# Optimization experiments

Hardware: AMD Instinct MI355X
Metric: run time of the kernel (lower is better)

The kernel has to match this reference:

```python
import jax, jax.numpy as jnp
import numpy as np

H = 512        # HIDDEN_SIZE
HEADS = 4      # MEM_HEAD
KDIM = 256     # K_DIM (= H//2), HEADS*KDIM == 2*H
HALF = KDIM // 2
KNN = 32
SUB = 512      # SUB_SIZE
MEM = SUB * SUB
BN_EPS = 1e-5


def setup_inputs() -> dict:
    key = jax.random.key(0)
    ks = jax.random.split(key, 6)
    x = jax.random.normal(ks[0], (32, 64, H), jnp.float32)
    w1 = jax.random.normal(ks[1], (H // 2, H), jnp.float32) / np.sqrt(H).astype(np.float32)
    b1 = jnp.zeros((H // 2,), jnp.float32)
    w2 = jax.random.normal(ks[2], (2 * H, H // 2), jnp.float32) / np.sqrt(H // 2).astype(np.float32)
    b2 = jnp.zeros((2 * H,), jnp.float32)
    bn_gamma = jnp.ones((KDIM,), jnp.float32)
    bn_beta = jnp.zeros((KDIM,), jnp.float32)
    keys = jax.random.normal(ks[3], (HEADS, 2, SUB, HALF), jnp.float32) / np.sqrt(HALF).astype(np.float32)
    values = jax.random.normal(ks[4], (MEM, H), jnp.float32) * (H ** -0.5)
    return dict(x=x, w1=w1, b1=b1, w2=w2, b2=b2,
                bn_gamma=bn_gamma, bn_beta=bn_beta, keys=keys, values=values)


def reference(x, w1, b1, w2, b2, bn_gamma, bn_beta, keys, values):
    B, L, _ = x.shape
    n = B * L
    # Query MLP: H -> H/2 -> 2H, viewed as (n, HEADS, KDIM)
    h = jax.nn.relu(jnp.einsum('blh,ch->blc', x, w1) + b1)
    q = jnp.einsum('blc,dc->bld', h, w2) + b2                      # (B, L, 2H)
    q = q.reshape(n, HEADS, KDIM)
    # BatchNorm1d over the K_DIM channel (training-mode batch stats)
    flat = q.reshape(-1, KDIM)
    mean = flat.mean(0)
    var = flat.var(0)
    q = (q - mean) * jax.lax.rsqrt(var + BN_EPS) * bn_gamma + bn_beta
    # Product-key double top-k
    q1, q2 = q[..., :HALF], q[..., HALF:]
    s1 = jnp.einsum('nhd,hkd->nhk', q1, keys[:, 0])                # (n, HEADS, SUB)
    s2 = jnp.einsum('nhd,hkd->nhk', q2, keys[:, 1])
    ts1, ti1 = jax.lax.top_k(s1, KNN)
    ts2, ti2 = jax.lax.top_k(s2, KNN)
    all_s = (ts1[..., :, None] + ts2[..., None, :]).reshape(n, HEADS, KNN * KNN)
    all_i = (ti1[..., :, None] * SUB + ti2[..., None, :]).reshape(n, HEADS, KNN * KNN)
    sc, best = jax.lax.top_k(all_s, KNN)                            # (n, HEADS, KNN)
    idx = jnp.take_along_axis(all_i, best, axis=-1)
    # Softmax over KNN within each head (scores viewed as (-1, KNN))
    w = jax.nn.softmax(sc, axis=-1)
    idx = idx.reshape(n, HEADS * KNN)
    w = w.reshape(n, HEADS * KNN)
    # EmbeddingBag(mode='sum') with per-sample weights
    out = jnp.einsum('nkh,nk->nh', values[idx], w)                  # (n, H)
    out = out.reshape(B, L, H)
    return out.sum(1)                                               # (B, H)
```

## Files before the change

### kernel.cpp

```cpp
#include <hip/hip_runtime.h>
#include <hip/hip_bf16.h>
#include <math.h>

#define N_TOK   2048
#define HDIM    512
#define HHALF   256
#define QDIM    1024
#define KDIM    256
#define HALF    128
#define HEADS   4
#define KNN     32
#define SUB     512
#define NROWS   8192

__device__ __forceinline__ void gemm_tile_nt(
    const float* __restrict__ A, int lda,
    const float* __restrict__ B, int ldb,
    float* __restrict__ C, int ldc,
    int K, const float* __restrict__ bias, bool relu,
    int m0, int n0)
{
    __shared__ float As[16][68];
    __shared__ float Bs[16][68];
    int tid = threadIdx.x;
    int tx = tid & 15;
    int ty = tid >> 4;
    int lr = tid >> 2;
    int lc = (tid & 3) * 4;

    float acc[4][4] = {};

    for (int k0 = 0; k0 < K; k0 += 16) {
        float4 a = *(const float4*)(A + (size_t)(m0 + lr) * lda + k0 + lc);
        float4 b = *(const float4*)(B + (size_t)(n0 + lr) * ldb + k0 + lc);
        As[lc + 0][lr] = a.x; As[lc + 1][lr] = a.y;
        As[lc + 2][lr] = a.z; As[lc + 3][lr] = a.w;
        Bs[lc + 0][lr] = b.x; Bs[lc + 1][lr] = b.y;
        Bs[lc + 2][lr] = b.z; Bs[lc + 3][lr] = b.w;
        __syncthreads();
#pragma unroll
        for (int k = 0; k < 16; ++k) {
            float4 av = *(const float4*)&As[k][ty * 4];
            float4 bv = *(const float4*)&Bs[k][tx * 4];
            acc[0][0] = fmaf(av.x, bv.x, acc[0][0]);
            acc[0][1] = fmaf(av.x, bv.y, acc[0][1]);
            acc[0][2] = fmaf(av.x, bv.z, acc[0][2]);
            acc[0][3] = fmaf(av.x, bv.w, acc[0][3]);
            acc[1][0] = fmaf(av.y, bv.x, acc[1][0]);
            acc[1][1] = fmaf(av.y, bv.y, acc[1][1]);
            acc[1][2] = fmaf(av.y, bv.z, acc[1][2]);
            acc[1][3] = fmaf(av.y, bv.w, acc[1][3]);
            acc[2][0] = fmaf(av.z, bv.x, acc[2][0]);
            acc[2][1] = fmaf(av.z, bv.y, acc[2][1]);
            acc[2][2] = fmaf(av.z, bv.z, acc[2][2]);
            acc[2][3] = fmaf(av.z, bv.w, acc[2][3]);
            acc[3][0] = fmaf(av.w, bv.x, acc[3][0]);
            acc[3][1] = fmaf(av.w, bv.y, acc[3][1]);
            acc[3][2] = fmaf(av.w, bv.z, acc[3][2]);
            acc[3][3] = fmaf(av.w, bv.w, acc[3][3]);
        }
        __syncthreads();
    }

    float4 bb = make_float4(0.f, 0.f, 0.f, 0.f);
    if (bias) {
        bb.x = bias[n0 + tx * 4 + 0];
        bb.y = bias[n0 + tx * 4 + 1];
        bb.z = bias[n0 + tx * 4 + 2];
        bb.w = bias[n0 + tx * 4 + 3];
    }
#pragma unroll
    for (int i = 0; i < 4; ++i) {
        int m = m0 + ty * 4 + i;
        float4 r;
        r.x = acc[i][0] + bb.x;
        r.y = acc[i][1] + bb.y;
        r.z = acc[i][2] + bb.z;
        r.w = acc[i][3] + bb.w;
        if (relu) {
            r.x = fmaxf(r.x, 0.f); r.y = fmaxf(r.y, 0.f);
            r.z = fmaxf(r.z, 0.f); r.w = fmaxf(r.w, 0.f);
        }
        *(float4*)(C + (size_t)m * ldc + n0 + tx * 4) = r;
    }
}

__global__ __launch_bounds__(256) void gemm_nt_kernel(
    const float* __restrict__ A, int lda,
    const float* __restrict__ B, int ldb,
    float* __restrict__ C, int ldc,
    int K, const float* __restrict__ bias, int relu)
{
    gemm_tile_nt(A, lda, B, ldb, C, ldc, K, bias, relu != 0,
                 blockIdx.x * 64, blockIdx.y * 64);
}

__global__ __launch_bounds__(256) void score_kernel(
    const float* __restrict__ q, const float* __restrict__ keys,
    float* __restrict__ s1, float* __restrict__ s2)
{
    int z = blockIdx.z;
    int hh = z >> 1;
    int half = z & 1;
    const float* A = q + hh * KDIM + half * HALF;
    const float* B = keys + (size_t)z * SUB * HALF;
    float* C = (half ? s2 : s1) + hh * SUB;
    gemm_tile_nt(A, QDIM, B, HALF, C, HEADS * SUB, HALF, nullptr, false,
                 blockIdx.x * 64, blockIdx.y * 64);
}

__global__ __launch_bounds__(256) void bnstat_kernel(
    const float* __restrict__ q, float* __restrict__ partial)
{
    int c = threadIdx.x;
    int b = blockIdx.x;
    const float* base = q + (size_t)b * 32 * KDIM;
    float s = 0.f, s2 = 0.f;
#pragma unroll 8
    for (int r = 0; r < 32; ++r) {
        float v = base[r * KDIM + c];
        s += v;
        s2 = fmaf(v, v, s2);
    }
    partial[b * KDIM + c] = s;
    partial[256 * KDIM + b * KDIM + c] = s2;
}

__global__ __launch_bounds__(256) void bnfinal_kernel(
    const float* __restrict__ partial,
    const float* __restrict__ gamma, const float* __restrict__ beta,
    float* __restrict__ scsh)
{
    int c = threadIdx.x;
    float s = 0.f, s2 = 0.f;
    for (int b = 0; b < 256; ++b) {
        s += partial[b * KDIM + c];
        s2 += partial[256 * KDIM + b * KDIM + c];
    }
    float mean = s * (1.f / (float)NROWS);
    float var = s2 * (1.f / (float)NROWS) - mean * mean;
    float rstd = rsqrtf(var + 1e-5f);
    float sc = rstd * gamma[c];
    scsh[c] = sc;
    scsh[KDIM + c] = beta[c] - mean * sc;
}

__global__ __launch_bounds__(256) void bnapply_kernel(
    float* __restrict__ q, const float* __restrict__ scsh)
{
    int c = threadIdx.x;
    float sc = scsh[c];
    float sh = scsh[KDIM + c];
    size_t base = (size_t)blockIdx.x * 1024 + c;
#pragma unroll
    for (int r = 0; r < 4; ++r) {
        float v = q[base + r * KDIM];
        q[base + r * KDIM] = fmaf(v, sc, sh);
    }
}

__global__ __launch_bounds__(64) void topk_kernel(
    const float* __restrict__ s1, const float* __restrict__ s2,
    int* __restrict__ out_idx, float* __restrict__ out_w)
{
    const float NEG = -3.0e38f;
    int task = blockIdx.x;
    int lane = threadIdx.x;
    __shared__ float ts1[KNN]; __shared__ int ti1[KNN];
    __shared__ float ts2[KNN]; __shared__ int ti2[KNN];
    __shared__ float scv[KNN]; __shared__ int scp[KNN];

    for (int src = 0; src < 2; ++src) {
        const float* base = (src ? s2 : s1) + (size_t)task * SUB;
        float v[8];
#pragma unroll
        for (int i = 0; i < 8; ++i) v[i] = base[lane + 64 * i];
        float* tsv = src ? ts2 : ts1;
        int*   tsi = src ? ti2 : ti1;
        for (int t = 0; t < KNN; ++t) {
            float best = v[0]; int bi = 0;
#pragma unroll
            for (int i = 1; i < 8; ++i)
                if (v[i] > best) { best = v[i]; bi = i; }
            float bv = best;
            int bg = lane + 64 * bi;
#pragma unroll
            for (int off = 32; off; off >>= 1) {
                float ov = __shfl_xor(bv, off);
                int og = __shfl_xor(bg, off);
                if (ov > bv || (ov == bv && og < bg)) { bv = ov; bg = og; }
            }
            if (lane == 0) { tsv[t] = bv; tsi[t] = bg; }
            if (lane == (bg & 63)) v[bg >> 6] = NEG;
        }
    }
    __syncthreads();

    float cv[16];
#pragma unroll
    for (int t = 0; t < 16; ++t) {
        int p = lane + 64 * t;
        cv[t] = ts1[p >> 5] + ts2[p & 31];
    }
    for (int t = 0; t < KNN; ++t) {
        float best = cv[0]; int bi = 0;
#pragma unroll
        for (int i = 1; i < 16; ++i)
            if (cv[i] > best) { best = cv[i]; bi = i; }
        float bv = best;
        int bp = lane + 64 * bi;
#pragma unroll
        for (int off = 32; off; off >>= 1) {
            float ov = __shfl_xor(bv, off);
            int op = __shfl_xor(bp, off);
            if (ov > bv || (ov == bv && op < bp)) { bv = ov; bp = op; }
        }
        if (lane == 0) { scv[t] = bv; scp[t] = bp; }
        if (lane == (bp & 63)) cv[bp >> 6] = NEG;
    }
    __syncthreads();

    float m = scv[0];
    float e = (lane < KNN) ? expf(scv[lane] - m) : 0.f;
    float ssum = e;
#pragma unroll
    for (int off = 32; off; off >>= 1) ssum += __shfl_xor(ssum, off);

    if (lane < KNN) {
        int p = scp[lane];
        int i = p >> 5, j = p & 31;
        int gidx = ti1[i] * SUB + ti2[j];
        int n = task >> 2, h = task & 3;
        out_idx[n * (HEADS * KNN) + h * KNN + lane] = gidx;
        out_w[n * (HEADS * KNN) + h * KNN + lane] = e / ssum;
    }
}

__global__ __launch_bounds__(256) void gather_kernel(
    const float* __restrict__ values, const int* __restrict__ idx,
    const float* __restrict__ w, float* __restrict__ rows)
{
    int n = blockIdx.x;
    int tid = threadIdx.x;
    __shared__ int sidx[HEADS * KNN];
    __shared__ float sw[HEADS * KNN];
    if (tid < HEADS * KNN) {
        sidx[tid] = idx[n * (HEADS * KNN) + tid];
        sw[tid] = w[n * (HEADS * KNN) + tid];
    }
    __syncthreads();
    const float2* vv = (const float2*)values;
    float2 acc = make_float2(0.f, 0.f);
#pragma unroll 4
    for (int k = 0; k < HEADS * KNN; ++k) {
        float2 v = vv[(size_t)sidx[k] * (HDIM / 2) + tid];
        float wk = sw[k];
        acc.x = fmaf(wk, v.x, acc.x);
        acc.y = fmaf(wk, v.y, acc.y);
    }
    ((float2*)rows)[(size_t)n * (HDIM / 2) + tid] = acc;
}

__global__ __launch_bounds__(512) void reduce_kernel(
    const float* __restrict__ rows, float* __restrict__ out)
{
    int b = blockIdx.x;
    int c = threadIdx.x;
    float s = 0.f;
    for (int l = 0; l < 64; ++l)
        s += rows[(size_t)(b * 64 + l) * HDIM + c];
    out[b * HDIM + c] = s;
}

extern "C" void kernel_launch(void* const* d_in, const int* in_sizes, int n_in,
                              void* d_out, int out_size, void* d_ws, size_t ws_size,
                              hipStream_t stream)
{
    const float* x      = (const float*)d_in[0];
    const float* w1     = (const float*)d_in[1];
    const float* b1     = (const float*)d_in[2];
    const float* w2     = (const float*)d_in[3];
    const float* b2     = (const float*)d_in[4];
    const float* gamma  = (const float*)d_in[5];
    const float* beta   = (const float*)d_in[6];
    const float* keys   = (const float*)d_in[7];
    const float* values = (const float*)d_in[8];
    float* out = (float*)d_out;

    float* ws = (float*)d_ws;
    float* h       = ws;
    float* q       = h + N_TOK * HHALF;
    float* partial = q + N_TOK * QDIM;
    float* scsh    = partial + 2 * 256 * KDIM;
    float* s1      = scsh + 2 * KDIM;
    float* s2      = s1 + (size_t)N_TOK * HEADS * SUB;
    int*   tidx    = (int*)(s2 + (size_t)N_TOK * HEADS * SUB);
    float* tw      = (float*)(tidx + N_TOK * HEADS * KNN);
    float* rows    = tw + N_TOK * HEADS * KNN;

    gemm_nt_kernel<<<dim3(N_TOK / 64, HHALF / 64), 256, 0, stream>>>(
        x, HDIM, w1, HDIM, h, HHALF, HDIM, b1, 1);

    gemm_nt_kernel<<<dim3(N_TOK / 64, QDIM / 64), 256, 0, stream>>>(
        h, HHALF, w2, HHALF, q, QDIM, HHALF, b2, 0);

    bnstat_kernel<<<256, 256, 0, stream>>>(q, partial);
    bnfinal_kernel<<<1, 256, 0, stream>>>(partial, gamma, beta, scsh);
    bnapply_kernel<<<N_TOK, 256, 0, stream>>>(q, scsh);

    score_kernel<<<dim3(N_TOK / 64, SUB / 64, HEADS * 2), 256, 0, stream>>>(
        q, keys, s1, s2);

    topk_kernel<<<N_TOK * HEADS, 64, 0, stream>>>(s1, s2, tidx, tw);

    gather_kernel<<<N_TOK, 256, 0, stream>>>(values, tidx, tw, rows);

    reduce_kernel<<<32, 512, 0, stream>>>(rows, out);
}
```

Measured before the change: 898.0 us.

## Replace iterative argmax top-k with radix-select threshold; widen gather loads to float4

```diff
diff --git a/kernel.cpp b/kernel.cpp
--- a/kernel.cpp
+++ b/kernel.cpp
@@ -159,77 +159,101 @@
     }
 }
 
-__global__ __launch_bounds__(64) void topk_kernel(
+__device__ __forceinline__ unsigned fmap(float f) {
+    unsigned u = __float_as_uint(f);
+    return (u & 0x80000000u) ? ~u : (u | 0x80000000u);
+}
+
+__device__ __forceinline__ int mbcnt64(unsigned long long m) {
+    return __builtin_amdgcn_mbcnt_hi((unsigned)(m >> 32),
+           __builtin_amdgcn_mbcnt_lo((unsigned)(m & 0xffffffffu), 0));
+}
+
+__global__ __launch_bounds__(256) void topk_kernel(
     const float* __restrict__ s1, const float* __restrict__ s2,
     int* __restrict__ out_idx, float* __restrict__ out_w)
 {
-    const float NEG = -3.0e38f;
-    int task = blockIdx.x;
-    int lane = threadIdx.x;
-    __shared__ float ts1[KNN]; __shared__ int ti1[KNN];
-    __shared__ float ts2[KNN]; __shared__ int ti2[KNN];
-    __shared__ float scv[KNN]; __shared__ int scp[KNN];
+    int w = threadIdx.x >> 6;
+    int lane = threadIdx.x & 63;
+    int task = blockIdx.x * 4 + w;
+
+    __shared__ float ts1[4][KNN]; __shared__ int ti1[4][KNN];
+    __shared__ float ts2[4][KNN]; __shared__ int ti2[4][KNN];
+    __shared__ float scv[4][KNN]; __shared__ int scp[4][KNN];
 
     for (int src = 0; src < 2; ++src) {
         const float* base = (src ? s2 : s1) + (size_t)task * SUB;
-        float v[8];
-#pragma unroll
-        for (int i = 0; i < 8; ++i) v[i] = base[lane + 64 * i];
-        float* tsv = src ? ts2 : ts1;
-        int*   tsi = src ? ti2 : ti1;
-        for (int t = 0; t < KNN; ++t) {
-            float best = v[0]; int bi = 0;
-#pragma unroll
-            for (int i = 1; i < 8; ++i)
-                if (v[i] > best) { best = v[i]; bi = i; }
-            float bv = best;
-            int bg = lane + 64 * bi;
-#pragma unroll
-            for (int off = 32; off; off >>= 1) {
-                float ov = __shfl_xor(bv, off);
-                int og = __shfl_xor(bg, off);
-                if (ov > bv || (ov == bv && og < bg)) { bv = ov; bg = og; }
+        float v[8]; unsigned u[8];
+#pragma unroll
+        for (int i = 0; i < 8; ++i) {
+            v[i] = base[lane + 64 * i];
+            u[i] = fmap(v[i]);
+        }
+        unsigned t = 0u;
+        for (int bit = 31; bit >= 0; --bit) {
+            unsigned cand = t | (1u << bit);
+            int cnt = 0;
+#pragma unroll
+            for (int i = 0; i < 8; ++i)
+                cnt += __popcll(__ballot(u[i] >= cand));
+            if (cnt >= KNN) t = cand;
+        }
+        float* tsv = src ? ts2[w] : ts1[w];
+        int*   tsi = src ? ti2[w] : ti1[w];
+        int pbase = 0;
+#pragma unroll
+        for (int i = 0; i < 8; ++i) {
+            unsigned long long m = __ballot(u[i] >= t);
+            if (u[i] >= t) {
+                int pos = pbase + mbcnt64(m);
+                if (pos < KNN) { tsv[pos] = v[i]; tsi[pos] = lane + 64 * i; }
             }
-            if (lane == 0) { tsv[t] = bv; tsi[t] = bg; }
-            if (lane == (bg & 63)) v[bg >> 6] = NEG;
+            pbase += __popcll(m);
         }
     }
     __syncthreads();
 
-    float cv[16];
-#pragma unroll
-    for (int t = 0; t < 16; ++t) {
-        int p = lane + 64 * t;
-        cv[t] = ts1[p >> 5] + ts2[p & 31];
-    }
-    for (int t = 0; t < KNN; ++t) {
-        float best = cv[0]; int bi = 0;
-#pragma unroll
-        for (int i = 1; i < 16; ++i)
-            if (cv[i] > best) { best = cv[i]; bi = i; }
-        float bv = best;
-        int bp = lane + 64 * bi;
-#pragma unroll
-        for (int off = 32; off; off >>= 1) {
-            float ov = __shfl_xor(bv, off);
-            int op = __shfl_xor(bp, off);
-            if (ov > bv || (ov == bv && op < bp)) { bv = ov; bp = op; }
-        }
-        if (lane == 0) { scv[t] = bv; scp[t] = bp; }
-        if (lane == (bp & 63)) cv[bp >> 6] = NEG;
+    float cv[16]; unsigned cu[16];
+#pragma unroll
+    for (int i = 0; i < 16; ++i) {
+        int p = lane + 64 * i;
+        cv[i] = ts1[w][p >> 5] + ts2[w][p & 31];
+        cu[i] = fmap(cv[i]);
+    }
+    unsigned t2 = 0u;
+    for (int bit = 31; bit >= 0; --bit) {
+        unsigned cand = t2 | (1u << bit);
+        int cnt = 0;
+#pragma unroll
+        for (int i = 0; i < 16; ++i)
+            cnt += __popcll(__ballot(cu[i] >= cand));
+        if (cnt >= KNN) t2 = cand;
+    }
+    int pbase = 0;
+#pragma unroll
+    for (int i = 0; i < 16; ++i) {
+        unsigned long long m = __ballot(cu[i] >= t2);
+        if (cu[i] >= t2) {
+            int pos = pbase + mbcnt64(m);
+            if (pos < KNN) { scv[w][pos] = cv[i]; scp[w][pos] = lane + 64 * i; }
+        }
+        pbase += __popcll(m);
     }
     __syncthreads();
 
-    float m = scv[0];
-    float e = (lane < KNN) ? expf(scv[lane] - m) : 0.f;
+    float x = (lane < KNN) ? scv[w][lane] : -3.0e38f;
+    float mx = x;
+#pragma unroll
+    for (int off = 32; off; off >>= 1) mx = fmaxf(mx, __shfl_xor(mx, off));
+    float e = (lane < KNN) ? expf(x - mx) : 0.f;
     float ssum = e;
 #pragma unroll
     for (int off = 32; off; off >>= 1) ssum += __shfl_xor(ssum, off);
 
     if (lane < KNN) {
-        int p = scp[lane];
+        int p = scp[w][lane];
         int i = p >> 5, j = p & 31;
-        int gidx = ti1[i] * SUB + ti2[j];
+        int gidx = ti1[w][i] * SUB + ti2[w][j];
         int n = task >> 2, h = task & 3;
         out_idx[n * (HEADS * KNN) + h * KNN + lane] = gidx;
         out_w[n * (HEADS * KNN) + h * KNN + lane] = e / ssum;
@@ -242,23 +266,34 @@
 {
     int n = blockIdx.x;
     int tid = threadIdx.x;
+    int pair = tid >> 7;
+    int c4 = tid & 127;
     __shared__ int sidx[HEADS * KNN];
     __shared__ float sw[HEADS * KNN];
+    __shared__ float4 tmp[128];
     if (tid < HEADS * KNN) {
         sidx[tid] = idx[n * (HEADS * KNN) + tid];
         sw[tid] = w[n * (HEADS * KNN) + tid];
     }
     __syncthreads();
-    const float2* vv = (const float2*)values;
-    float2 acc = make_float2(0.f, 0.f);
-#pragma unroll 4
-    for (int k = 0; k < HEADS * KNN; ++k) {
-        float2 v = vv[(size_t)sidx[k] * (HDIM / 2) + tid];
+    const float4* vv = (const float4*)values;
+    float4 acc = make_float4(0.f, 0.f, 0.f, 0.f);
+#pragma unroll 8
+    for (int k = pair; k < HEADS * KNN; k += 2) {
+        float4 v = vv[(size_t)sidx[k] * (HDIM / 4) + c4];
         float wk = sw[k];
         acc.x = fmaf(wk, v.x, acc.x);
         acc.y = fmaf(wk, v.y, acc.y);
-    }
-    ((float2*)rows)[(size_t)n * (HDIM / 2) + tid] = acc;
+        acc.z = fmaf(wk, v.z, acc.z);
+        acc.w = fmaf(wk, v.w, acc.w);
+    }
+    if (pair) tmp[c4] = acc;
+    __syncthreads();
+    if (!pair) {
+        float4 o = tmp[c4];
+        acc.x += o.x; acc.y += o.y; acc.z += o.z; acc.w += o.w;
+        ((float4*)rows)[(size_t)n * (HDIM / 4) + c4] = acc;
+    }
 }
 
 __global__ __launch_bounds__(512) void reduce_kernel(
@@ -311,7 +346,7 @@
     score_kernel<<<dim3(N_TOK / 64, SUB / 64, HEADS * 2), 256, 0, stream>>>(
         q, keys, s1, s2);
 
-    topk_kernel<<<N_TOK * HEADS, 64, 0, stream>>>(s1, s2, tidx, tw);
+    topk_kernel<<<N_TOK * HEADS / 4, 256, 0, stream>>>(s1, s2, tidx, tw);
 
     gather_kernel<<<N_TOK, 256, 0, stream>>>(values, tidx, tw, rows);
 
```

Result: faster. 796.5 us (-11.3%).
